# Performance work log

Hardware: AMD Instinct MI355X
Metric: run time of the kernel (lower is better)

## Reference

```python
import jax, jax.numpy as jnp
import numpy as np

B, T, C, HS = 256, 256, 384, 64


def setup_inputs() -> dict:
    key = jax.random.key(0)
    k1, k2, k3, k4 = jax.random.split(key, 4)
    X = jax.random.normal(k1, (B, T, C), dtype=jnp.float32)
    Wq = jax.random.normal(k2, (C, HS), dtype=jnp.float32) * (C ** -0.5)
    Wk = jax.random.normal(k3, (C, HS), dtype=jnp.float32) * (C ** -0.5)
    Wv = jax.random.normal(k4, (C, HS), dtype=jnp.float32) * (C ** -0.5)
    return {"X": X, "Wq": Wq, "Wk": Wk, "Wv": Wv}


def reference(X, Wq, Wk, Wv):
    # Single causal self-attention head (dropout in eval mode / identity).
    num_channels = X.shape[-1]
    q = jnp.einsum('btc,ch->bth', X, Wq)  # [B,T,HS]
    k = jnp.einsum('btc,ch->bth', X, Wk)
    v = jnp.einsum('btc,ch->bth', X, Wv)
    # NOTE: original scales by embedding dim C**-0.5, not head_size**-0.5.
    scores = jnp.einsum('bqh,bkh->bqk', q, k) * (num_channels ** -0.5)  # [B,T,T]
    Tq = X.shape[1]
    causal = jnp.tril(jnp.ones((Tq, Tq), dtype=bool))
    scores = jnp.where(causal, scores, jnp.float32(-jnp.inf))
    weights = jax.nn.softmax(scores, axis=-1)
    return jnp.einsum('bqk,bkh->bqh', weights, v)  # [B,T,HS]
```

## Files before the change

kernel.cpp:

```cpp
#include <hip/hip_runtime.h>
#include <hip/hip_bf16.h>

#define B_  256
#define T_  256
#define C_  384
#define HS_ 64
#define BT_ (B_*T_)

typedef __attribute__((ext_vector_type(8))) short short8;
typedef __attribute__((ext_vector_type(4))) float f32x4;

__device__ __forceinline__ unsigned short f2bf(float f) {
    unsigned u = __float_as_uint(f);
    u += 0x7FFFu + ((u >> 16) & 1u);
    return (unsigned short)(u >> 16);
}

__global__ __launch_bounds__(256) void prep_wfrag(
    const float* __restrict__ Wq, const float* __restrict__ Wk,
    const float* __restrict__ Wv, unsigned short* __restrict__ Wfrag)
{
    const int tid  = blockIdx.x * 256 + threadIdx.x;
    const int lane = tid & 63;
    const int q    = tid >> 6;
    const int f    = q % 3;
    const int q2   = q / 3;
    const int wn   = q2 & 3;
    const int s    = q2 >> 2;

    const int n     = wn * 48 + f * 16 + (lane & 15);
    const int kbase = s * 32 + (lane >> 4) * 8;
    const float* src = (n < 64) ? Wq : (n < 128) ? Wk : Wv;
    const int c      = n & 63;
    const float scale = (n < 64) ? 0.05103103630798288f : 1.0f;

    short8 out;
    #pragma unroll
    for (int j = 0; j < 8; ++j)
        out[j] = (short)f2bf(src[(size_t)(kbase + j) * HS_ + c] * scale);
    *(short8*)&Wfrag[(size_t)tid * 8] = out;
}

#define LQ_OFF 0
#define LK_OFF 18432
#define LV_OFF 36864
#define LX_OFF 53760
#define LDSP   40

__global__ __launch_bounds__(1024, 4) void head_fused(
    const float* __restrict__ X, const unsigned short* __restrict__ Wfrag,
    float* __restrict__ out)
{
    __shared__ unsigned short lds[74240];
    const int t    = threadIdx.x;
    const int w    = t >> 6;
    const int lane = t & 63;
    const int lo   = lane & 15;
    const int hi   = lane >> 4;
    const int b    = blockIdx.x;
    const int wm   = w >> 2, wn = w & 3;

    const float* Xb = X + (size_t)b * T_ * C_;
    const short8* Wf = (const short8*)Wfrag;

    const int srow  = t >> 2;
    const int squad = t & 3;

    auto stage_load = [&](int k0, float4* g) {
        const float* p = Xb + (size_t)srow * C_ + k0 + squad * 8;
        g[0] = *(const float4*)(p);
        g[1] = *(const float4*)(p + 4);
    };
    auto stage_write = [&](int buf, const float4* g) {
        short8 p;
        p[0] = (short)f2bf(g[0].x); p[1] = (short)f2bf(g[0].y);
        p[2] = (short)f2bf(g[0].z); p[3] = (short)f2bf(g[0].w);
        p[4] = (short)f2bf(g[1].x); p[5] = (short)f2bf(g[1].y);
        p[6] = (short)f2bf(g[1].z); p[7] = (short)f2bf(g[1].w);
        *(short8*)&lds[LX_OFF + buf * 10240 + srow * 40 + squad * 8] = p;
    };
    auto load_w = [&](int s, short8* wf) {
        const short8* base = Wf + ((size_t)(s * 4 + wn) * 3) * 64 + lane;
        #pragma unroll
        for (int f = 0; f < 3; ++f)
            wf[f] = base[f * 64];
    };

    float4 g[2];
    short8 wf[3];
    stage_load(0, g);
    load_w(0, wf);
    stage_write(0, g);
    __syncthreads();

    f32x4 acc[4][3];
    #pragma unroll
    for (int m = 0; m < 4; ++m)
        #pragma unroll
        for (int f = 0; f < 3; ++f)
            acc[m][f] = (f32x4){0.f, 0.f, 0.f, 0.f};

    #pragma unroll 2
    for (int s = 0; s < 12; ++s) {
        const int cur = s & 1;
        float4 gn[2];
        short8 wfn[3];
        if (s < 11) {
            stage_load((s + 1) * 32, gn);
            load_w(s + 1, wfn);
        }
        short8 af[4];
        #pragma unroll
        for (int m = 0; m < 4; ++m)
            af[m] = *(const short8*)&lds[LX_OFF + cur * 10240 + (wm * 64 + m * 16 + lo) * 40 + hi * 8];
        #pragma unroll
        for (int m = 0; m < 4; ++m)
            #pragma unroll
            for (int f = 0; f < 3; ++f)
                acc[m][f] = __builtin_amdgcn_mfma_f32_16x16x32_bf16(af[m], wf[f], acc[m][f], 0, 0, 0);
        if (s < 11) {
            stage_write(cur ^ 1, gn);
            wf[0] = wfn[0]; wf[1] = wfn[1]; wf[2] = wfn[2];
        }
        __syncthreads();
    }

    #pragma unroll
    for (int m = 0; m < 4; ++m) {
        const int rowb = wm * 64 + m * 16 + hi * 4;
        #pragma unroll
        for (int f = 0; f < 3; ++f) {
            const int base = wn * 48 + f * 16;
            if (base < 64) {
                #pragma unroll
                for (int r = 0; r < 4; ++r)
                    lds[LQ_OFF + (rowb + r) * 72 + base + lo] = f2bf(acc[m][f][r]);
            } else if (base < 128) {
                #pragma unroll
                for (int r = 0; r < 4; ++r)
                    lds[LK_OFF + (rowb + r) * 72 + (base - 64) + lo] = f2bf(acc[m][f][r]);
            } else {
                ushort4 pk = { f2bf(acc[m][f][0]), f2bf(acc[m][f][1]),
                               f2bf(acc[m][f][2]), f2bf(acc[m][f][3]) };
                *(ushort4*)&lds[LV_OFF + (base - 128 + lo) * 264 + rowb] = pk;
            }
        }
    }
    __syncthreads();

    unsigned short* Pw = &lds[LX_OFF + w * 640];

    const int sg  = w & 3, pos = w >> 2;
    const int tq  = (pos == 0) ? sg : (pos == 1) ? 15 - sg : (pos == 2) ? 4 + sg : 11 - sg;

    {
        short8 qf0 = *(const short8*)&lds[LQ_OFF + (tq * 16 + lo) * 72 + hi * 8];
        short8 qf1 = *(const short8*)&lds[LQ_OFF + (tq * 16 + lo) * 72 + hi * 8 + 32];

        f32x4 acc_o[4];
        #pragma unroll
        for (int n = 0; n < 4; ++n) acc_o[n] = (f32x4){0.f, 0.f, 0.f, 0.f};
        float Mr[4] = {-1e30f, -1e30f, -1e30f, -1e30f};
        float Lr[4] = {0.f, 0.f, 0.f, 0.f};

        const int nsteps = (tq >> 1) + 1;
        for (int s = 0; s < nsteps; ++s) {
            const int kv0 = s * 32;
            f32x4 sa[2];
            sa[0] = (f32x4){0.f, 0.f, 0.f, 0.f};
            sa[1] = (f32x4){0.f, 0.f, 0.f, 0.f};
            #pragma unroll
            for (int n = 0; n < 2; ++n) {
                const unsigned short* kb = &lds[LK_OFF + (kv0 + n * 16 + lo) * 72 + hi * 8];
                short8 kf0 = *(const short8*)kb;
                short8 kf1 = *(const short8*)(kb + 32);
                sa[n] = __builtin_amdgcn_mfma_f32_16x16x32_bf16(qf0, kf0, sa[n], 0, 0, 0);
                sa[n] = __builtin_amdgcn_mfma_f32_16x16x32_bf16(qf1, kf1, sa[n], 0, 0, 0);
            }
            if (s == nsteps - 1) {
                #pragma unroll
                for (int n = 0; n < 2; ++n)
                    #pragma unroll
                    for (int r = 0; r < 4; ++r) {
                        int kv = kv0 + n * 16 + lo;
                        int q  = tq * 16 + hi * 4 + r;
                        if (kv > q) sa[n][r] = -1e30f;
                    }
            }
            #pragma unroll
            for (int r = 0; r < 4; ++r) {
                float m = fmaxf(sa[0][r], sa[1][r]);
                m = fmaxf(m, __shfl_xor(m, 1));
                m = fmaxf(m, __shfl_xor(m, 2));
                m = fmaxf(m, __shfl_xor(m, 4));
                m = fmaxf(m, __shfl_xor(m, 8));
                float Mn = fmaxf(Mr[r], m);
                float fr = __expf(Mr[r] - Mn);
                Mr[r] = Mn;
                float p0 = __expf(sa[0][r] - Mn);
                float p1 = __expf(sa[1][r] - Mn);
                float ls = p0 + p1;
                ls += __shfl_xor(ls, 1);
                ls += __shfl_xor(ls, 2);
                ls += __shfl_xor(ls, 4);
                ls += __shfl_xor(ls, 8);
                Lr[r] = Lr[r] * fr + ls;
                #pragma unroll
                for (int n = 0; n < 4; ++n) acc_o[n][r] *= fr;
                Pw[(hi * 4 + r) * LDSP + lo]      = f2bf(p0);
                Pw[(hi * 4 + r) * LDSP + 16 + lo] = f2bf(p1);
            }
            short8 pf = *(const short8*)&Pw[lo * LDSP + hi * 8];
            #pragma unroll
            for (int n = 0; n < 4; ++n) {
                short8 vf = *(const short8*)&lds[LV_OFF + (n * 16 + lo) * 264 + kv0 + hi * 8];
                acc_o[n] = __builtin_amdgcn_mfma_f32_16x16x32_bf16(pf, vf, acc_o[n], 0, 0, 0);
            }
        }
        #pragma unroll
        for (int r = 0; r < 4; ++r) {
            float inv = 1.0f / Lr[r];
            float* op = out + ((size_t)(b * 256 + tq * 16 + hi * 4 + r)) * HS_ + lo;
            #pragma unroll
            for (int n = 0; n < 4; ++n)
                op[n * 16] = acc_o[n][r] * inv;
        }
    }
}

extern "C" void kernel_launch(void* const* d_in, const int* in_sizes, int n_in,
                              void* d_out, int out_size, void* d_ws, size_t ws_size,
                              hipStream_t stream) {
    const float* X  = (const float*)d_in[0];
    const float* Wq = (const float*)d_in[1];
    const float* Wk = (const float*)d_in[2];
    const float* Wv = (const float*)d_in[3];
    float* out = (float*)d_out;

    unsigned short* Wfrag = (unsigned short*)d_ws;

    prep_wfrag<<<36, 256, 0, stream>>>(Wq, Wk, Wv, Wfrag);
    head_fused<<<B_, 1024, 0, stream>>>(X, Wfrag, out);
}
```

Before: 41.30 us.

## Transpose attention MFMAs so each lane owns one query row

Swaps the MFMA operand order in the attention loop to compute S^T and O^T, so each lane holds a single query row's scores across registers. The softmax row max and sum then need only two cross-lane shuffles instead of four per row, with one running max and one running sum per lane. P is written to LDS as vectorized ushort4 stores rather than scalar stores. The output write pattern changes to contiguous per-lane rows, which alters how global stores coalesce.

```diff
diff --git a/kernel.cpp b/kernel.cpp
--- a/kernel.cpp
+++ b/kernel.cpp
@@ -154,77 +154,74 @@
     const int tq  = (pos == 0) ? sg : (pos == 1) ? 15 - sg : (pos == 2) ? 4 + sg : 11 - sg;
 
     {
-        short8 qf0 = *(const short8*)&lds[LQ_OFF + (tq * 16 + lo) * 72 + hi * 8];
-        short8 qf1 = *(const short8*)&lds[LQ_OFF + (tq * 16 + lo) * 72 + hi * 8 + 32];
+        const int q_lane = tq * 16 + lo;
+        short8 qf0 = *(const short8*)&lds[LQ_OFF + q_lane * 72 + hi * 8];
+        short8 qf1 = *(const short8*)&lds[LQ_OFF + q_lane * 72 + hi * 8 + 32];
 
         f32x4 acc_o[4];
         #pragma unroll
         for (int n = 0; n < 4; ++n) acc_o[n] = (f32x4){0.f, 0.f, 0.f, 0.f};
-        float Mr[4] = {-1e30f, -1e30f, -1e30f, -1e30f};
-        float Lr[4] = {0.f, 0.f, 0.f, 0.f};
+        float Mr = -1e30f, Lr = 0.f;
 
         const int nsteps = (tq >> 1) + 1;
         for (int s = 0; s < nsteps; ++s) {
             const int kv0 = s * 32;
-            f32x4 sa[2];
-            sa[0] = (f32x4){0.f, 0.f, 0.f, 0.f};
-            sa[1] = (f32x4){0.f, 0.f, 0.f, 0.f};
+            f32x4 sb[2];
+            sb[0] = (f32x4){0.f, 0.f, 0.f, 0.f};
+            sb[1] = (f32x4){0.f, 0.f, 0.f, 0.f};
             #pragma unroll
             for (int n = 0; n < 2; ++n) {
                 const unsigned short* kb = &lds[LK_OFF + (kv0 + n * 16 + lo) * 72 + hi * 8];
                 short8 kf0 = *(const short8*)kb;
                 short8 kf1 = *(const short8*)(kb + 32);
-                sa[n] = __builtin_amdgcn_mfma_f32_16x16x32_bf16(qf0, kf0, sa[n], 0, 0, 0);
-                sa[n] = __builtin_amdgcn_mfma_f32_16x16x32_bf16(qf1, kf1, sa[n], 0, 0, 0);
+                sb[n] = __builtin_amdgcn_mfma_f32_16x16x32_bf16(kf0, qf0, sb[n], 0, 0, 0);
+                sb[n] = __builtin_amdgcn_mfma_f32_16x16x32_bf16(kf1, qf1, sb[n], 0, 0, 0);
             }
             if (s == nsteps - 1) {
                 #pragma unroll
                 for (int n = 0; n < 2; ++n)
                     #pragma unroll
-                    for (int r = 0; r < 4; ++r) {
-                        int kv = kv0 + n * 16 + lo;
-                        int q  = tq * 16 + hi * 4 + r;
-                        if (kv > q) sa[n][r] = -1e30f;
-                    }
-            }
-            #pragma unroll
-            for (int r = 0; r < 4; ++r) {
-                float m = fmaxf(sa[0][r], sa[1][r]);
-                m = fmaxf(m, __shfl_xor(m, 1));
-                m = fmaxf(m, __shfl_xor(m, 2));
-                m = fmaxf(m, __shfl_xor(m, 4));
-                m = fmaxf(m, __shfl_xor(m, 8));
-                float Mn = fmaxf(Mr[r], m);
-                float fr = __expf(Mr[r] - Mn);
-                Mr[r] = Mn;
-                float p0 = __expf(sa[0][r] - Mn);
-                float p1 = __expf(sa[1][r] - Mn);
-                float ls = p0 + p1;
-                ls += __shfl_xor(ls, 1);
-                ls += __shfl_xor(ls, 2);
-                ls += __shfl_xor(ls, 4);
-                ls += __shfl_xor(ls, 8);
-                Lr[r] = Lr[r] * fr + ls;
-                #pragma unroll
-                for (int n = 0; n < 4; ++n) acc_o[n][r] *= fr;
-                Pw[(hi * 4 + r) * LDSP + lo]      = f2bf(p0);
-                Pw[(hi * 4 + r) * LDSP + 16 + lo] = f2bf(p1);
-            }
+                    for (int r = 0; r < 4; ++r)
+                        if (kv0 + n * 16 + hi * 4 + r > q_lane) sb[n][r] = -1e30f;
+            }
+            float pmax = fmaxf(fmaxf(fmaxf(sb[0][0], sb[0][1]), fmaxf(sb[0][2], sb[0][3])),
+                               fmaxf(fmaxf(sb[1][0], sb[1][1]), fmaxf(sb[1][2], sb[1][3])));
+            pmax = fmaxf(pmax, __shfl_xor(pmax, 16));
+            pmax = fmaxf(pmax, __shfl_xor(pmax, 32));
+            const float Mn = fmaxf(Mr, pmax);
+            const float fr = __expf(Mr - Mn);
+            Mr = Mn;
+            float p0 = __expf(sb[0][0] - Mn), p1 = __expf(sb[0][1] - Mn);
+            float p2 = __expf(sb[0][2] - Mn), p3 = __expf(sb[0][3] - Mn);
+            float p4 = __expf(sb[1][0] - Mn), p5 = __expf(sb[1][1] - Mn);
+            float p6 = __expf(sb[1][2] - Mn), p7 = __expf(sb[1][3] - Mn);
+            float ls = ((p0 + p1) + (p2 + p3)) + ((p4 + p5) + (p6 + p7));
+            ls += __shfl_xor(ls, 16);
+            ls += __shfl_xor(ls, 32);
+            Lr = Lr * fr + ls;
+            #pragma unroll
+            for (int n = 0; n < 4; ++n) {
+                acc_o[n][0] *= fr; acc_o[n][1] *= fr;
+                acc_o[n][2] *= fr; acc_o[n][3] *= fr;
+            }
+            ushort4 w0 = { f2bf(p0), f2bf(p1), f2bf(p2), f2bf(p3) };
+            ushort4 w1 = { f2bf(p4), f2bf(p5), f2bf(p6), f2bf(p7) };
+            *(ushort4*)&Pw[lo * LDSP + hi * 4]      = w0;
+            *(ushort4*)&Pw[lo * LDSP + 16 + hi * 4] = w1;
             short8 pf = *(const short8*)&Pw[lo * LDSP + hi * 8];
             #pragma unroll
             for (int n = 0; n < 4; ++n) {
                 short8 vf = *(const short8*)&lds[LV_OFF + (n * 16 + lo) * 264 + kv0 + hi * 8];
-                acc_o[n] = __builtin_amdgcn_mfma_f32_16x16x32_bf16(pf, vf, acc_o[n], 0, 0, 0);
-            }
-        }
-        #pragma unroll
-        for (int r = 0; r < 4; ++r) {
-            float inv = 1.0f / Lr[r];
-            float* op = out + ((size_t)(b * 256 + tq * 16 + hi * 4 + r)) * HS_ + lo;
-            #pragma unroll
-            for (int n = 0; n < 4; ++n)
-                op[n * 16] = acc_o[n][r] * inv;
-        }
+                acc_o[n] = __builtin_amdgcn_mfma_f32_16x16x32_bf16(vf, pf, acc_o[n], 0, 0, 0);
+            }
+        }
+        const float inv = 1.0f / Lr;
+        float* op = out + ((size_t)(b * 256 + q_lane)) * HS_;
+        #pragma unroll
+        for (int n = 0; n < 4; ++n)
+            #pragma unroll
+            for (int r = 0; r < 4; ++r)
+                op[n * 16 + hi * 4 + r] = acc_o[n][r] * inv;
     }
 }
 
```

After: 36.47 us. -11.7%, faster.
